# Optimization experiments

Measured on AMD Instinct MI355X. Metric: run time of the kernel, lower is better.

## Reference

```python
import jax, jax.numpy as jnp
import numpy as np
import math

# Config (matches init_kwargs)
B, IMG, NP, PS = 32, 224, 14, 16
P = PS * PS              # flattened patch dim = 256
D, NH, L, C = 768, 12, 12, 1000
DQ = D // NH             # 64
S = NP * NP + 1          # 197 tokens (cls + patches)
MLP_H = 4 * D
EPS = 1e-5


def positional_embeddings(seq_len, d):
    i = jnp.arange(seq_len, dtype=jnp.float32)[:, None]
    j = jnp.arange(d, dtype=jnp.float32)[None, :]
    even = jnp.sin(i / 10000.0 ** (j / d))
    odd = jnp.cos(i / 10000.0 ** ((j - 1.0) / d))
    return jnp.where(jnp.arange(d)[None, :] % 2 == 0, even, odd)


def layernorm(x, g, b):
    mu = jnp.mean(x, axis=-1, keepdims=True)
    var = jnp.mean((x - mu) ** 2, axis=-1, keepdims=True)
    return (x - mu) * jax.lax.rsqrt(var + EPS) * g + b


def setup_inputs() -> dict:
    key = jax.random.key(0)
    ks = jax.random.split(key, 24)
    s = 0.02
    return {
        "X": jax.random.normal(ks[0], (B, IMG, IMG), jnp.float32),
        "patch_W": jax.random.normal(ks[1], (P, D), jnp.float32) * s,
        "patch_b": jnp.zeros((D,), jnp.float32),
        "cls_token": jax.random.uniform(ks[2], (1, D), jnp.float32),
        "ln1_g": jnp.ones((L, D), jnp.float32),
        "ln1_b": jnp.zeros((L, D), jnp.float32),
        "Wq": jax.random.normal(ks[3], (L, NH, D, DQ), jnp.float32) * s,
        "bq": jnp.zeros((L, NH, DQ), jnp.float32),
        "Wk": jax.random.normal(ks[4], (L, NH, D, DQ), jnp.float32) * s,
        "bk": jnp.zeros((L, NH, DQ), jnp.float32),
        "Wv": jax.random.normal(ks[5], (L, NH, D, DQ), jnp.float32) * s,
        "bv": jnp.zeros((L, NH, DQ), jnp.float32),
        "proj_W": jax.random.normal(ks[6], (L, D, D), jnp.float32) * s,
        "proj_b": jnp.zeros((L, D), jnp.float32),
        "ln2_g": jnp.ones((L, D), jnp.float32),
        "ln2_b": jnp.zeros((L, D), jnp.float32),
        "mlp_W1": jax.random.normal(ks[7], (L, D, MLP_H), jnp.float32) * s,
        "mlp_b1": jnp.zeros((L, MLP_H), jnp.float32),
        "mlp_W2": jax.random.normal(ks[8], (L, MLP_H, D), jnp.float32) * s,
        "mlp_b2": jnp.zeros((L, D), jnp.float32),
        "head_W": jax.random.normal(ks[9], (D, C), jnp.float32) * s,
        "head_b": jnp.zeros((C,), jnp.float32),
    }


def _forward(X, patch_W, patch_b, cls_token, ln1_g, ln1_b, Wq, bq, Wk, bk, Wv, bv,
             proj_W, proj_b, ln2_g, ln2_b, mlp_W1, mlp_b1, mlp_W2, mlp_b2,
             head_W, head_b):
    b = X.shape[0]
    # patchify: (B,H,W) -> (B, NP*NP, PS*PS)
    patches = X.reshape(b, NP, PS, NP, PS).transpose(0, 1, 3, 2, 4).reshape(b, NP * NP, P)
    tok = patches @ patch_W + patch_b                      # (B, NP^2, D)
    cls = jnp.broadcast_to(cls_token[None], (b, 1, D))
    x = jnp.concatenate([cls, tok], axis=1)                # (B, S, D)
    x = x + positional_embeddings(S, D)[None]
    scale = 1.0 / math.sqrt(DQ)
    for l in range(L):
        n1 = layernorm(x, ln1_g[l], ln1_b[l])
        q = jnp.einsum("bsd,hde->bhse", n1, Wq[l]) + bq[l][None, :, None, :]
        k = jnp.einsum("bsd,hde->bhse", n1, Wk[l]) + bk[l][None, :, None, :]
        v = jnp.einsum("bsd,hde->bhse", n1, Wv[l]) + bv[l][None, :, None, :]
        att = jax.nn.softmax(jnp.einsum("bhse,bhte->bhst", q, k) * scale, axis=-1)
        o = jnp.einsum("bhst,bhte->bhse", att, v)          # (B,NH,S,DQ)
        o = o.transpose(0, 2, 1, 3).reshape(b, S, D)       # hstack heads
        x = x + o @ proj_W[l] + proj_b[l]
        n2 = layernorm(x, ln2_g[l], ln2_b[l])
        h = jax.nn.gelu(n2 @ mlp_W1[l] + mlp_b1[l], approximate=False)
        x = x + h @ mlp_W2[l] + mlp_b2[l]
    return x[:, 0] @ head_W + head_b                       # (B, C)


def reference(X, patch_W, patch_b, cls_token, ln1_g, ln1_b, Wq, bq, Wk, bk, Wv, bv,
              proj_W, proj_b, ln2_g, ln2_b, mlp_W1, mlp_b1, mlp_W2, mlp_b2,
              head_W, head_b):
    return _forward(X, patch_W, patch_b, cls_token, ln1_g, ln1_b, Wq, bq, Wk, bk,
                    Wv, bv, proj_W, proj_b, ln2_g, ln2_b, mlp_W1, mlp_b1,
                    mlp_W2, mlp_b2, head_W, head_b)
```

## Files before the change

kernel.cpp:

```cpp
#include <hip/hip_runtime.h>
#include <hip/hip_bf16.h>
#include <math.h>
#include <stdint.h>

#define VB   32
#define VS   197
#define VD   768
#define VNH  12
#define VDQ  64
#define VL   12
#define VMLP 3072
#define VC   1000
#define VP   256
#define VNPAT 196
#define VTOK (VB * VS)
#define TOKD ((size_t)VTOK * VD)

typedef __attribute__((ext_vector_type(4))) float f32x4;
typedef __attribute__((ext_vector_type(8))) short short8;

typedef __attribute__((address_space(1))) const unsigned int GU;
typedef __attribute__((address_space(3))) unsigned int LU;

__device__ __forceinline__ void gload_lds16(const void* g, void* l) {
    __builtin_amdgcn_global_load_lds((GU*)(uintptr_t)g, (LU*)(uintptr_t)l, 16, 0, 0);
}

__device__ __forceinline__ void xcd_swz(int gx, int gy, int& bx, int& by) {
    int nwg = gx * gy;
    int hw = by * gx + bx;
    int q = nwg >> 3, r = nwg & 7;
    int xcd = hw & 7, off = hw >> 3;
    int lid = (xcd < r ? xcd * (q + 1) : r * (q + 1) + (xcd - r) * q) + off;
    bx = lid % gx; by = lid / gx;
}

__device__ __forceinline__ float gelu_f(float x) {
    float t = 0.7978845608f * x * fmaf(0.044715f, x * x, 1.0f);
    float a = fminf(t * 2.8853900818f, 80.0f);
    float e = __builtin_amdgcn_exp2f(a);
    return x * e * __builtin_amdgcn_rcpf(1.0f + e);
}

__global__ void patchify_k(const float* __restrict__ X, __hip_bfloat16* __restrict__ P) {
    int idx = blockIdx.x * 256 + threadIdx.x;
    const int total = VB * VNPAT * VP;
    if (idx >= total) return;
    int i  = idx & 255;
    int p  = (idx >> 8) % VNPAT;
    int b  = (idx >> 8) / VNPAT;
    int pr = p / 14, pc = p % 14;
    int a  = i >> 4, c2 = i & 15;
    P[idx] = __float2bfloat16(X[((size_t)b * 224 + pr * 16 + a) * 224 + pc * 16 + c2]);
}

__global__ void pos_cls_k(float* __restrict__ x, const float* __restrict__ cls) {
    size_t idx = (size_t)blockIdx.x * 256 + threadIdx.x;
    if (idx >= TOKD) return;
    int j = (int)(idx % VD);
    int s = (int)((idx / VD) % VS);
    float jj = (float)(j & ~1);
    float freq = expf(-(jj / (float)VD) * 9.2103403719761836f);
    float ang  = (float)s * freq;
    float pe   = (j & 1) ? cosf(ang) : sinf(ang);
    if (s == 0) x[idx] = cls[j] + pe;
    else        x[idx] += pe;
}

__global__ __launch_bounds__(256) void layernorm_k(
    const float* __restrict__ x, __hip_bfloat16* __restrict__ y,
    const float* __restrict__ g, const float* __restrict__ bta)
{
    int t = blockIdx.x;
    const float* xr = x + (size_t)t * VD;
    __hip_bfloat16* yr = y + (size_t)t * VD;
    int tid = threadIdx.x;
    float v[3];
    float s = 0.f;
    #pragma unroll
    for (int i = 0; i < 3; i++) { v[i] = xr[tid + i * 256]; s += v[i]; }
    __shared__ float red[8];
    #pragma unroll
    for (int off = 32; off; off >>= 1) s += __shfl_xor(s, off);
    int lane = tid & 63, w = tid >> 6;
    if (!lane) red[w] = s;
    __syncthreads();
    float mu = (red[0] + red[1] + red[2] + red[3]) * (1.f / VD);
    float s2 = 0.f;
    #pragma unroll
    for (int i = 0; i < 3; i++) { float d0 = v[i] - mu; s2 += d0 * d0; }
    #pragma unroll
    for (int off = 32; off; off >>= 1) s2 += __shfl_xor(s2, off);
    if (!lane) red[4 + w] = s2;
    __syncthreads();
    float var = (red[4] + red[5] + red[6] + red[7]) * (1.f / VD);
    float rs = rsqrtf(var + 1e-5f);
    #pragma unroll
    for (int i = 0; i < 3; i++) {
        int j = tid + i * 256;
        yr[j] = __float2bfloat16((v[i] - mu) * rs * g[j] + bta[j]);
    }
}

template<int DO_LN>
__global__ __launch_bounds__(256) void combineln_k(
    float* __restrict__ x, const float* __restrict__ p0, const float* __restrict__ p1,
    const float* __restrict__ bias, const float* __restrict__ g,
    const float* __restrict__ bta, __hip_bfloat16* __restrict__ y)
{
    int t = blockIdx.x;
    size_t base = (size_t)t * VD;
    int tid = threadIdx.x;
    float v[3];
    float s = 0.f;
    #pragma unroll
    for (int i = 0; i < 3; i++) {
        int j = tid + i * 256;
        float val = x[base + j] + p0[base + j] + p1[base + j] + bias[j];
        x[base + j] = val;
        v[i] = val; s += val;
    }
    if (DO_LN) {
        __shared__ float red[8];
        #pragma unroll
        for (int off = 32; off; off >>= 1) s += __shfl_xor(s, off);
        int lane = tid & 63, w = tid >> 6;
        if (!lane) red[w] = s;
        __syncthreads();
        float mu = (red[0] + red[1] + red[2] + red[3]) * (1.f / VD);
        float s2 = 0.f;
        #pragma unroll
        for (int i = 0; i < 3; i++) { float d0 = v[i] - mu; s2 += d0 * d0; }
        #pragma unroll
        for (int off = 32; off; off >>= 1) s2 += __shfl_xor(s2, off);
        if (!lane) red[4 + w] = s2;
        __syncthreads();
        float var = (red[4] + red[5] + red[6] + red[7]) * (1.f / VD);
        float rs = rsqrtf(var + 1e-5f);
        #pragma unroll
        for (int i = 0; i < 3; i++) {
            int j = tid + i * 256;
            y[base + j] = __float2bfloat16((v[i] - mu) * rs * g[j] + bta[j]);
        }
    }
}

__global__ __launch_bounds__(256) void tpose_k(
    const float* __restrict__ in, __hip_bfloat16* __restrict__ out, int R, int C)
{
    __shared__ float t[32][33];
    int c0 = blockIdx.x * 32, r0 = blockIdx.y * 32;
    int tc = threadIdx.x & 31, tr = threadIdx.x >> 5;
    #pragma unroll
    for (int p = 0; p < 4; p++) {
        int r = r0 + tr + p * 8;
        t[tr + p * 8][tc] = (r < R && c0 + tc < C) ? in[(size_t)r * C + c0 + tc] : 0.f;
    }
    __syncthreads();
    #pragma unroll
    for (int p = 0; p < 4; p++) {
        int c = c0 + tr + p * 8;
        if (c < C && r0 + tc < R)
            out[(size_t)c * R + r0 + tc] = __float2bfloat16(t[tc][tr + p * 8]);
    }
}

#define OFF_PROJ (2304 * 768)
#define OFF_M1   (OFF_PROJ + 768 * 768)
#define OFF_M2   (OFF_M1 + 3072 * 768)

__device__ __forceinline__ unsigned pack2bf(float a, float b) {
    __hip_bfloat16 x = __float2bfloat16(a), y = __float2bfloat16(b);
    unsigned short ux = *(unsigned short*)&x, uy = *(unsigned short*)&y;
    return (unsigned)ux | ((unsigned)uy << 16);
}

__global__ __launch_bounds__(256) void wprep_k(
    const float* __restrict__ Wq, const float* __restrict__ Wk,
    const float* __restrict__ Wv, const float* __restrict__ Wp,
    const float* __restrict__ W1, const float* __restrict__ W2,
    __hip_bfloat16* __restrict__ wT)
{
    __shared__ float t[32][33];
    int z = blockIdx.x;
    const float* src; __hip_bfloat16* dst;
    int C, ldd, r0, c0;
    if (z < 1728) {
        int head = z / 48, tt = z % 48;
        int m = head / VNH, h = head % VNH;
        src = (m == 0 ? Wq : m == 1 ? Wk : Wv) + (size_t)h * VD * VDQ;
        dst = wT + ((size_t)m * VD + h * VDQ) * VD;
        C = VDQ; ldd = VD;
        r0 = (tt >> 1) * 32; c0 = (tt & 1) * 32;
    } else if (z < 2304) {
        int z2 = z - 1728;
        src = Wp; dst = wT + OFF_PROJ;
        C = VD; ldd = VD;
        r0 = (z2 / 24) * 32; c0 = (z2 % 24) * 32;
    } else if (z < 4608) {
        int z3 = z - 2304;
        src = W1; dst = wT + OFF_M1;
        C = VMLP; ldd = VD;
        r0 = (z3 / 96) * 32; c0 = (z3 % 96) * 32;
    } else {
        int z4 = z - 4608;
        src = W2; dst = wT + OFF_M2;
        C = VD; ldd = VMLP;
        r0 = (z4 / 24) * 32; c0 = (z4 % 24) * 32;
    }
    int tid = threadIdx.x;
    {
        int r = tid >> 3, cq = (tid & 7) << 2;
        float4 v = *(const float4*)&src[(size_t)(r0 + r) * C + c0 + cq];
        t[r][cq] = v.x; t[r][cq + 1] = v.y; t[r][cq + 2] = v.z; t[r][cq + 3] = v.w;
    }
    __syncthreads();
    {
        int c = tid >> 3, rq = (tid & 7) << 2;
        unsigned u0 = pack2bf(t[rq][c],     t[rq + 1][c]);
        unsigned u1 = pack2bf(t[rq + 2][c], t[rq + 3][c]);
        unsigned* dp = (unsigned*)&dst[(size_t)(c0 + c) * ldd + r0 + rq];
        dp[0] = u0; dp[1] = u1;
    }
}

__global__ void cball_k(const float* __restrict__ bq, const float* __restrict__ bk,
                        const float* __restrict__ bv, float* __restrict__ cb) {
    int idx = blockIdx.x * 256 + threadIdx.x;
    if (idx >= VL * 3 * VD) return;
    int l = idx / (3 * VD), n = idx % (3 * VD);
    int m = n / VD, wi = n % VD;
    const float* p = (m == 0) ? bq : (m == 1) ? bk : bv;
    cb[idx] = p[l * VD + wi];
}

__global__ void cls_k(const float* __restrict__ x, __hip_bfloat16* __restrict__ out) {
    int idx = blockIdx.x * 256 + threadIdx.x;
    if (idx >= VB * VD) return;
    int b = idx / VD, d = idx % VD;
    out[idx] = __float2bfloat16(x[(size_t)b * VS * VD + d]);
}

template<int EPI>
__global__ __launch_bounds__(256) void bgemm_k(
    const __hip_bfloat16* __restrict__ A,
    const __hip_bfloat16* __restrict__ BT,
    const float* __restrict__ bias,
    void* __restrict__ Co,
    int M, int K, int ldc, int Ncols)
{
    __shared__ short A_s[128][64];
    __shared__ short B_s[128][64];
    int bx = blockIdx.x, by = blockIdx.y;
    xcd_swz(gridDim.x, gridDim.y, bx, by);
    const int tid = threadIdx.x;
    const int w = tid >> 6, l = tid & 63;
    const int row0 = by * 128, col0 = bx * 128;
    const int wm = (w >> 1) << 6, wn = (w & 1) << 6;
    f32x4 acc[4][4] = {};

    const int lr = l >> 3;
    const int sslot = (l & 7) ^ lr;
    int arow[4], brow[4];
    #pragma unroll
    for (int i = 0; i < 4; i++) {
        int r = (4 * w + i) * 8 + lr;
        arow[i] = min(row0 + r, M - 1);
        brow[i] = min(col0 + r, Ncols - 1);
    }
    for (int k0 = 0; k0 < K; k0 += 64) {
        __syncthreads();
        #pragma unroll
        for (int i = 0; i < 4; i++) {
            int ch = 4 * w + i;
            gload_lds16((const void*)(A + (size_t)arow[i] * K + k0 + (sslot << 3)),
                        (void*)(&A_s[ch * 8][0]));
            gload_lds16((const void*)(BT + (size_t)brow[i] * K + k0 + (sslot << 3)),
                        (void*)(&B_s[ch * 8][0]));
        }
        __syncthreads();
        #pragma unroll
        for (int ks = 0; ks < 2; ks++) {
            const int s16 = (ks << 2) + (l >> 4);
            short8 av[4], bv[4];
            #pragma unroll
            for (int i = 0; i < 4; i++) {
                int ar = wm + i * 16 + (l & 15);
                av[i] = *(const short8*)((const char*)&A_s[ar][0] + ((s16 ^ (ar & 7)) << 4));
                int br = wn + i * 16 + (l & 15);
                bv[i] = *(const short8*)((const char*)&B_s[br][0] + ((s16 ^ (br & 7)) << 4));
            }
            #pragma unroll
            for (int i = 0; i < 4; i++)
                #pragma unroll
                for (int j = 0; j < 4; j++)
                    acc[i][j] = __builtin_amdgcn_mfma_f32_16x16x32_bf16(av[i], bv[j], acc[i][j], 0, 0, 0);
        }
    }
    const int rbase = row0 + wm + ((l >> 4) << 2);
    const int cbase = col0 + wn + (l & 15);
    #pragma unroll
    for (int i = 0; i < 4; i++) {
        #pragma unroll
        for (int q = 0; q < 4; q++) {
            int rr = rbase + i * 16 + q;
            if (rr >= M) continue;
            #pragma unroll
            for (int j = 0; j < 4; j++) {
                int c = cbase + j * 16;
                if (c >= Ncols) continue;
                float v = acc[i][j][q] + bias[c];
                if (EPI == 0) {
                    int orow = rr + rr / VNPAT + 1;
                    ((float*)Co)[(size_t)orow * ldc + c] = v;
                } else if (EPI == 1) {
                    ((__hip_bfloat16*)Co)[(size_t)rr * ldc + c] = __float2bfloat16(v);
                } else if (EPI == 2) {
                    ((float*)Co)[(size_t)rr * ldc + c] += v;
                } else if (EPI == 3) {
                    ((__hip_bfloat16*)Co)[(size_t)rr * ldc + c] = __float2bfloat16(gelu_f(v));
                } else {
                    ((float*)Co)[(size_t)rr * ldc + c] = v;
                }
            }
        }
    }
}

template<int EPI>
__global__ __launch_bounds__(512) void bgemm8_k(
    const __hip_bfloat16* __restrict__ A,
    const __hip_bfloat16* __restrict__ BT,
    const float* __restrict__ bias,
    __hip_bfloat16* __restrict__ Co,
    int M, int K, int ldc)
{
    __shared__ short SA[3][256][32];
    __shared__ short SB[3][256][32];
    const int tid = threadIdx.x;
    const int w = tid >> 6, l = tid & 63;
    const int fr = l & 15, g = l >> 4;
    const int wr = w >> 2, wc = w & 3;
    const int row0 = blockIdx.y * 256, col0 = blockIdx.x * 256;
    f32x4 acc[8][4] = {};

    const int sr = tid >> 2;
    const int sslot = (tid & 3) ^ ((sr >> 1) & 3);
    const __hip_bfloat16* aS[2]; const __hip_bfloat16* bS[2];
    #pragma unroll
    for (int u = 0; u < 2; u++) {
        aS[u] = A  + (size_t)min(row0 + u * 128 + sr, M - 1) * K + sslot * 8;
        bS[u] = BT + (size_t)(col0 + u * 128 + sr) * K + sslot * 8;
    }
    const int doff = sr * 64 + (tid & 3) * 16;

    #define STG_A(ring, t) { const int k0 = (t) << 5;                          \
        gload_lds16(aS[0] + k0, (char*)&SA[ring][0][0] + doff);                \
        gload_lds16(aS[1] + k0, (char*)&SA[ring][0][0] + 8192 + doff); }
    #define STG_B(ring, t) { const int k0 = (t) << 5;                          \
        gload_lds16(bS[0] + k0, (char*)&SB[ring][0][0] + doff);                \
        gload_lds16(bS[1] + k0, (char*)&SB[ring][0][0] + 8192 + doff); }

    const int nt = K >> 5;
    STG_A(0, 0); STG_B(0, 0);
    STG_A(1, 1); STG_B(1, 1);
    asm volatile("s_waitcnt vmcnt(4)" ::: "memory");
    __builtin_amdgcn_s_barrier();

    short8 breg[4];
    for (int t = 0; t < nt; t++) {
        const int ring = t % 3;
        const int rs   = (t + 2) % 3;
        const char* sa = (const char*)&SA[ring][0][0];
        const char* sb = (const char*)&SB[ring][0][0];
        short8 areg[4];
        #pragma unroll
        for (int n = 0; n < 4; n++) {
            int br = wc * 64 + n * 16 + fr;
            breg[n] = *(const short8*)(sb + br * 64 + ((g ^ ((br >> 1) & 3)) << 4));
        }
        #pragma unroll
        for (int m = 0; m < 4; m++) {
            int ar = wr * 128 + m * 16 + fr;
            areg[m] = *(const short8*)(sa + ar * 64 + ((g ^ ((ar >> 1) & 3)) << 4));
        }
        if (t + 2 < nt) STG_A(rs, t + 2);
        __builtin_amdgcn_s_barrier();
        asm volatile("s_waitcnt lgkmcnt(0)" ::: "memory");
        __builtin_amdgcn_sched_barrier(0);
        __builtin_amdgcn_s_setprio(1);
        #pragma unroll
        for (int m = 0; m < 4; m++)
            #pragma unroll
            for (int n = 0; n < 4; n++)
                acc[m][n] = __builtin_amdgcn_mfma_f32_16x16x32_bf16(areg[m], breg[n], acc[m][n], 0, 0, 0);
        __builtin_amdgcn_s_setprio(0);
        __builtin_amdgcn_s_barrier();
        #pragma unroll
        for (int m = 0; m < 4; m++) {
            int ar = wr * 128 + (m + 4) * 16 + fr;
            areg[m] = *(const short8*)(sa + ar * 64 + ((g ^ ((ar >> 1) & 3)) << 4));
        }
        if (t + 2 < nt) STG_B(rs, t + 2);
        __builtin_amdgcn_s_barrier();
        asm volatile("s_waitcnt lgkmcnt(0)" ::: "memory");
        __builtin_amdgcn_sched_barrier(0);
        __builtin_amdgcn_s_setprio(1);
        #pragma unroll
        for (int m = 0; m < 4; m++)
            #pragma unroll
            for (int n = 0; n < 4; n++)
                acc[m + 4][n] = __builtin_amdgcn_mfma_f32_16x16x32_bf16(areg[m], breg[n], acc[m + 4][n], 0, 0, 0);
        __builtin_amdgcn_s_setprio(0);
        if (t + 2 < nt) {
            asm volatile("s_waitcnt vmcnt(4)" ::: "memory");
            __builtin_amdgcn_s_barrier();
        } else if (t + 1 < nt) {
            asm volatile("s_waitcnt vmcnt(0)" ::: "memory");
            __builtin_amdgcn_s_barrier();
        }
    }
    #undef STG_A
    #undef STG_B

    const int rb = row0 + wr * 128 + (g << 2);
    const int cb = col0 + wc * 64 + fr;
    #pragma unroll
    for (int m = 0; m < 8; m++) {
        #pragma unroll
        for (int q = 0; q < 4; q++) {
            int rr = rb + m * 16 + q;
            if (rr >= M) continue;
            #pragma unroll
            for (int n = 0; n < 4; n++) {
                int c = cb + n * 16;
                float v = acc[m][n][q] + bias[c];
                if (EPI == 3) v = gelu_f(v);
                Co[(size_t)rr * ldc + c] = __float2bfloat16(v);
            }
        }
    }
}

__global__ __launch_bounds__(256) void bgemm5_k(
    const __hip_bfloat16* __restrict__ A,
    const __hip_bfloat16* __restrict__ BT,
    float* __restrict__ P,
    int M, int K, int ldc)
{
    __shared__ short A_s[128][64];
    __shared__ short B_s[128][64];
    int bx = blockIdx.x, by = blockIdx.y;
    xcd_swz(gridDim.x, gridDim.y, bx, by);
    const int ks = blockIdx.z;
    const int khalf = K >> 1;
    const __hip_bfloat16* Ab  = A  + (size_t)ks * khalf;
    const __hip_bfloat16* BTb = BT + (size_t)ks * khalf;
    float* Pb = P + (size_t)ks * TOKD;

    const int tid = threadIdx.x;
    const int w = tid >> 6, l = tid & 63;
    const int row0 = by * 128, col0 = bx * 128;
    const int wm = (w >> 1) << 6, wn = (w & 1) << 6;
    f32x4 acc[4][4] = {};

    const int lr = l >> 3;
    const int sslot = (l & 7) ^ lr;
    int arow[4], brow[4];
    #pragma unroll
    for (int i = 0; i < 4; i++) {
        int r = (4 * w + i) * 8 + lr;
        arow[i] = min(row0 + r, M - 1);
        brow[i] = col0 + r;
    }
    for (int k0 = 0; k0 < khalf; k0 += 64) {
        __syncthreads();
        #pragma unroll
        for (int i = 0; i < 4; i++) {
            int ch = 4 * w + i;
            gload_lds16((const void*)(Ab + (size_t)arow[i] * K + k0 + (sslot << 3)),
                        (void*)(&A_s[ch * 8][0]));
            gload_lds16((const void*)(BTb + (size_t)brow[i] * K + k0 + (sslot << 3)),
                        (void*)(&B_s[ch * 8][0]));
        }
        __syncthreads();
        #pragma unroll
        for (int ks2 = 0; ks2 < 2; ks2++) {
            const int s16 = (ks2 << 2) + (l >> 4);
            short8 av[4], bv[4];
            #pragma unroll
            for (int i = 0; i < 4; i++) {
                int ar = wm + i * 16 + (l & 15);
                av[i] = *(const short8*)((const char*)&A_s[ar][0] + ((s16 ^ (ar & 7)) << 4));
                int br = wn + i * 16 + (l & 15);
                bv[i] = *(const short8*)((const char*)&B_s[br][0] + ((s16 ^ (br & 7)) << 4));
            }
            #pragma unroll
            for (int i = 0; i < 4; i++)
                #pragma unroll
                for (int j = 0; j < 4; j++)
                    acc[i][j] = __builtin_amdgcn_mfma_f32_16x16x32_bf16(av[i], bv[j], acc[i][j], 0, 0, 0);
        }
    }
    const int rbase = row0 + wm + ((l >> 4) << 2);
    const int cbase = col0 + wn + (l & 15);
    #pragma unroll
    for (int i = 0; i < 4; i++) {
        #pragma unroll
        for (int q = 0; q < 4; q++) {
            int rr = rbase + i * 16 + q;
            if (rr >= M) continue;
            #pragma unroll
            for (int j = 0; j < 4; j++) {
                int c = cbase + j * 16;
                Pb[(size_t)rr * ldc + c] = acc[i][j][q];
            }
        }
    }
}

__device__ __forceinline__ int swz_idx(int row, int k) {
    return row * 256 + (((k >> 3) ^ (row & 7)) << 3) + (k & 7);
}

__global__ __launch_bounds__(256) void attn3_k(
    const __hip_bfloat16* __restrict__ qkv, __hip_bfloat16* __restrict__ o)
{
    __shared__ short V_t[64 * 256];
    __shared__ short P_s[4][16 * 256];
    const int half = blockIdx.x;
    const int bh = blockIdx.y;
    const int b = bh / VNH, h = bh % VNH;
    const int tid = threadIdx.x, w = tid >> 6, l = tid & 63;
    const int g = l >> 4, c16 = l & 15;

    const __hip_bfloat16* base = qkv + (size_t)(b * VS) * (3 * VD) + h * VDQ;

    {
        const __hip_bfloat16* vbase = base + 2 * VD;
        int t = tid & 31, e0 = (tid >> 5) * 8;
        #pragma unroll
        for (int it = 0; it < 7; it++) {
            int tt = it * 32 + t;
            if (tt < VS) {
                short8 vv = *(const short8*)(vbase + (size_t)tt * (3 * VD) + e0);
                #pragma unroll
                for (int j = 0; j < 8; j++) V_t[swz_idx(e0 + j, tt)] = vv[j];
            }
        }
        for (int idx = tid; idx < 64 * 27; idx += 256) {
            int e = idx / 27, k = 197 + idx % 27;
            V_t[swz_idx(e, k)] = 0;
        }
    }
    {
        unsigned* p0 = (unsigned*)&P_s[w][swz_idx(c16, 208 + g * 4)];
        p0[0] = 0; p0[1] = 0;
    }
    __syncthreads();

    const int qt_end = half ? 13 : 7;
    for (int qt = 7 * half + w; qt < qt_end; qt += 4) {
        const int q0 = qt * 16;
        int qr = min(q0 + c16, VS - 1);
        const __hip_bfloat16* qp = base + (size_t)qr * (3 * VD) + g * 8;
        short8 qa0 = *(const short8*)(qp);
        short8 qa1 = *(const short8*)(qp + 32);

        f32x4 st[13];
        __builtin_amdgcn_s_setprio(1);
        #pragma unroll
        for (int t = 0; t < 13; t++) {
            int kr = min(t * 16 + c16, VS - 1);
            const __hip_bfloat16* kp = base + VD + (size_t)kr * (3 * VD) + g * 8;
            short8 ka0 = *(const short8*)(kp);
            short8 ka1 = *(const short8*)(kp + 32);
            f32x4 z = {};
            z = __builtin_amdgcn_mfma_f32_16x16x32_bf16(ka0, qa0, z, 0, 0, 0);
            z = __builtin_amdgcn_mfma_f32_16x16x32_bf16(ka1, qa1, z, 0, 0, 0);
            st[t] = z;
        }
        __builtin_amdgcn_s_setprio(0);
        #pragma unroll
        for (int t = 0; t < 13; t++) {
            #pragma unroll
            for (int r = 0; r < 4; r++) {
                float v = st[t][r] * 0.125f;
                if (t == 12 && (4 * g + r) >= 5) v = -3.0e38f;
                st[t][r] = v;
            }
        }
        float m = -3.0e38f;
        #pragma unroll
        for (int t = 0; t < 13; t++)
            #pragma unroll
            for (int r = 0; r < 4; r++) m = fmaxf(m, st[t][r]);
        m = fmaxf(m, __shfl_xor(m, 16));
        m = fmaxf(m, __shfl_xor(m, 32));
        float sum = 0.f;
        #pragma unroll
        for (int t = 0; t < 13; t++)
            #pragma unroll
            for (int r = 0; r < 4; r++) { float e = expf(st[t][r] - m); st[t][r] = e; sum += e; }
        sum += __shfl_xor(sum, 16);
        sum += __shfl_xor(sum, 32);
        float inv = 1.f / sum;
        #pragma unroll
        for (int t = 0; t < 13; t++) {
            int k0 = 16 * t + 4 * g;
            unsigned* pp = (unsigned*)&P_s[w][swz_idx(c16, k0)];
            pp[0] = pack2bf(st[t][0] * inv, st[t][1] * inv);
            pp[1] = pack2bf(st[t][2] * inv, st[t][3] * inv);
        }
        f32x4 acc[4] = {};
        __builtin_amdgcn_s_setprio(1);
        #pragma unroll
        for (int ki = 0; ki < 7; ki++) {
            int k0 = ki * 32 + g * 8;
            short8 pa = *(const short8*)&P_s[w][swz_idx(c16, k0)];
            #pragma unroll
            for (int et = 0; et < 4; et++) {
                short8 vbf = *(const short8*)&V_t[swz_idx(et * 16 + c16, k0)];
                acc[et] = __builtin_amdgcn_mfma_f32_16x16x32_bf16(pa, vbf, acc[et], 0, 0, 0);
            }
        }
        __builtin_amdgcn_s_setprio(0);
        #pragma unroll
        for (int et = 0; et < 4; et++) {
            #pragma unroll
            for (int r = 0; r < 4; r++) {
                int q = q0 + 4 * g + r;
                if (q < VS)
                    o[((size_t)(b * VS) + q) * VD + h * VDQ + et * 16 + c16] =
                        __float2bfloat16(acc[et][r]);
            }
        }
    }
}

extern "C" void kernel_launch(void* const* d_in, const int* in_sizes, int n_in,
                              void* d_out, int out_size, void* d_ws, size_t ws_size,
                              hipStream_t stream) {
    (void)in_sizes; (void)n_in; (void)out_size; (void)ws_size;
    const float* X       = (const float*)d_in[0];
    const float* patch_W = (const float*)d_in[1];
    const float* patch_b = (const float*)d_in[2];
    const float* cls_tok = (const float*)d_in[3];
    const float* ln1_g   = (const float*)d_in[4];
    const float* ln1_b   = (const float*)d_in[5];
    const float* Wq      = (const float*)d_in[6];
    const float* bq      = (const float*)d_in[7];
    const float* Wk      = (const float*)d_in[8];
    const float* bk      = (const float*)d_in[9];
    const float* Wv      = (const float*)d_in[10];
    const float* bv      = (const float*)d_in[11];
    const float* proj_W  = (const float*)d_in[12];
    const float* proj_b  = (const float*)d_in[13];
    const float* ln2_g   = (const float*)d_in[14];
    const float* ln2_b   = (const float*)d_in[15];
    const float* mlp_W1  = (const float*)d_in[16];
    const float* mlp_b1  = (const float*)d_in[17];
    const float* mlp_W2  = (const float*)d_in[18];
    const float* mlp_b2  = (const float*)d_in[19];
    const float* head_W  = (const float*)d_in[20];
    const float* head_b  = (const float*)d_in[21];

    char* ws = (char*)d_ws;
    float*          x    = (float*)ws;
    __hip_bfloat16* tb   = (__hip_bfloat16*)(ws + 19365888);
    __hip_bfloat16* big  = (__hip_bfloat16*)(ws + 29048832);
    __hip_bfloat16* wT   = (__hip_bfloat16*)(ws + 67780608);
    float*          cbA  = (float*)(ws + 81936384);
    float*          pbuf = (float*)(ws + 82046976);

    cball_k<<<(VL * 3 * VD + 255) / 256, 256, 0, stream>>>(bq, bk, bv, cbA);

    patchify_k<<<(VB * VNPAT * VP + 255) / 256, 256, 0, stream>>>(X, big);
    {
        dim3 g(VD / 32, VP / 32);
        tpose_k<<<g, 256, 0, stream>>>(patch_W, wT, VP, VD);
    }
    {
        dim3 g(VD / 128, VB * VNPAT / 128);
        bgemm_k<0><<<g, 256, 0, stream>>>(big, wT, patch_b, x, VB * VNPAT, VP, VD, VD);
    }
    pos_cls_k<<<(unsigned)((TOKD + 255) / 256), 256, 0, stream>>>(x, cls_tok);

    const size_t WSZ = (size_t)VNH * VD * VDQ;
    for (int l = 0; l < VL; l++) {
        wprep_k<<<6912, 256, 0, stream>>>(
            Wq + l * WSZ, Wk + l * WSZ, Wv + l * WSZ,
            proj_W + (size_t)l * VD * VD,
            mlp_W1 + (size_t)l * VD * VMLP,
            mlp_W2 + (size_t)l * VMLP * VD, wT);

        if (l == 0)
            layernorm_k<<<VTOK, 256, 0, stream>>>(x, tb, ln1_g, ln1_b);

        {
            dim3 g(3 * VD / 256, (VTOK + 255) / 256);
            bgemm8_k<1><<<g, 512, 0, stream>>>(tb, wT, cbA + l * 3 * VD, big,
                                               VTOK, VD, 3 * VD);
        }
        {
            dim3 ga(2, VB * VNH);
            attn3_k<<<ga, 256, 0, stream>>>(big, tb);
        }
        {
            dim3 g(VD / 128, (VTOK + 127) / 128, 2);
            bgemm5_k<<<g, 256, 0, stream>>>(tb, wT + OFF_PROJ, pbuf, VTOK, VD, VD);
            combineln_k<1><<<VTOK, 256, 0, stream>>>(
                x, pbuf, pbuf + TOKD, proj_b + l * VD,
                ln2_g + l * VD, ln2_b + l * VD, tb);
        }
        {
            dim3 g(VMLP / 256, (VTOK + 255) / 256);
            bgemm8_k<3><<<g, 512, 0, stream>>>(tb, wT + OFF_M1, mlp_b1 + l * VMLP, big,
                                               VTOK, VD, VMLP);
        }
        {
            dim3 g(VD / 128, (VTOK + 127) / 128, 2);
            bgemm5_k<<<g, 256, 0, stream>>>(big, wT + OFF_M2, pbuf, VTOK, VMLP, VD);
            if (l + 1 < VL)
                combineln_k<1><<<VTOK, 256, 0, stream>>>(
                    x, pbuf, pbuf + TOKD, mlp_b2 + l * VD,
                    ln1_g + (l + 1) * VD, ln1_b + (l + 1) * VD, tb);
            else
                combineln_k<0><<<VTOK, 256, 0, stream>>>(
                    x, pbuf, pbuf + TOKD, mlp_b2 + l * VD,
                    nullptr, nullptr, nullptr);
        }
    }
    cls_k<<<(VB * VD + 255) / 256, 256, 0, stream>>>(x, tb);
    {
        dim3 gt((VC + 31) / 32, VD / 32);
        tpose_k<<<gt, 256, 0, stream>>>(head_W, wT, VD, VC);
        dim3 g((VC + 127) / 128, 1);
        bgemm_k<4><<<g, 256, 0, stream>>>(tb, wT, head_b, (float*)d_out,
                                          VB, VD, VC, VC);
    }
}
```

Before: 3.125 ms.

## Pipeline split-K GEMM with triple-buffered LDS ring and trim bgemm8 barriers

Replaces the single-buffered split-K GEMM used for the projection and MLP-down layers with a 3-stage ring of 32-wide K tiles, prefetched two steps ahead through direct global-to-LDS loads. A vmcnt-gated barrier replaces the two __syncthreads per step, so memory loads overlap MFMA work. Separately, three intra-iteration s_barriers are removed from the bgemm8 main loop to cut synchronisation stalls. Dropping those barriers relies on the ring spacing keeping LDS reads and writes apart, which adds a risk of races.

```diff
diff --git a/kernel.cpp b/kernel.cpp
--- a/kernel.cpp
+++ b/kernel.cpp
@@ -385,7 +385,6 @@
             areg[m] = *(const short8*)(sa + ar * 64 + ((g ^ ((ar >> 1) & 3)) << 4));
         }
         if (t + 2 < nt) STG_A(rs, t + 2);
-        __builtin_amdgcn_s_barrier();
         asm volatile("s_waitcnt lgkmcnt(0)" ::: "memory");
         __builtin_amdgcn_sched_barrier(0);
         __builtin_amdgcn_s_setprio(1);
@@ -395,14 +394,12 @@
             for (int n = 0; n < 4; n++)
                 acc[m][n] = __builtin_amdgcn_mfma_f32_16x16x32_bf16(areg[m], breg[n], acc[m][n], 0, 0, 0);
         __builtin_amdgcn_s_setprio(0);
-        __builtin_amdgcn_s_barrier();
         #pragma unroll
         for (int m = 0; m < 4; m++) {
             int ar = wr * 128 + (m + 4) * 16 + fr;
             areg[m] = *(const short8*)(sa + ar * 64 + ((g ^ ((ar >> 1) & 3)) << 4));
         }
         if (t + 2 < nt) STG_B(rs, t + 2);
-        __builtin_amdgcn_s_barrier();
         asm volatile("s_waitcnt lgkmcnt(0)" ::: "memory");
         __builtin_amdgcn_sched_barrier(0);
         __builtin_amdgcn_s_setprio(1);
@@ -442,14 +439,14 @@
     }
 }
 
-__global__ __launch_bounds__(256) void bgemm5_k(
+__global__ __launch_bounds__(256) void bgemm9_k(
     const __hip_bfloat16* __restrict__ A,
     const __hip_bfloat16* __restrict__ BT,
     float* __restrict__ P,
     int M, int K, int ldc)
 {
-    __shared__ short A_s[128][64];
-    __shared__ short B_s[128][64];
+    __shared__ short SA[3][128][32];
+    __shared__ short SB[3][128][32];
     int bx = blockIdx.x, by = blockIdx.y;
     xcd_swz(gridDim.x, gridDim.y, bx, by);
     const int ks = blockIdx.z;
@@ -460,50 +457,70 @@
 
     const int tid = threadIdx.x;
     const int w = tid >> 6, l = tid & 63;
+    const int fr = l & 15, g = l >> 4;
     const int row0 = by * 128, col0 = bx * 128;
     const int wm = (w >> 1) << 6, wn = (w & 1) << 6;
     f32x4 acc[4][4] = {};
 
-    const int lr = l >> 3;
-    const int sslot = (l & 7) ^ lr;
-    int arow[4], brow[4];
-    #pragma unroll
-    for (int i = 0; i < 4; i++) {
-        int r = (4 * w + i) * 8 + lr;
-        arow[i] = min(row0 + r, M - 1);
-        brow[i] = col0 + r;
-    }
-    for (int k0 = 0; k0 < khalf; k0 += 64) {
-        __syncthreads();
+    const __hip_bfloat16* aS[2]; const __hip_bfloat16* bS[2];
+    int doff[2];
+    #pragma unroll
+    for (int q = 0; q < 2; q++) {
+        int idx = tid + (q << 8);
+        int r = idx >> 2;
+        int s = (idx & 3) ^ ((r >> 1) & 3);
+        aS[q] = Ab  + (size_t)min(row0 + r, M - 1) * K + s * 8;
+        bS[q] = BTb + (size_t)(col0 + r) * K + s * 8;
+        doff[q] = idx << 4;
+    }
+
+    #define STG9(ring, t) { const int k0 = (t) << 5;                           \
+        gload_lds16(aS[0] + k0, (char*)&SA[ring][0][0] + doff[0]);             \
+        gload_lds16(aS[1] + k0, (char*)&SA[ring][0][0] + doff[1]);             \
+        gload_lds16(bS[0] + k0, (char*)&SB[ring][0][0] + doff[0]);             \
+        gload_lds16(bS[1] + k0, (char*)&SB[ring][0][0] + doff[1]); }
+
+    const int nt = khalf >> 5;
+    STG9(0, 0);
+    STG9(1, 1);
+    asm volatile("s_waitcnt vmcnt(4)" ::: "memory");
+    __builtin_amdgcn_s_barrier();
+
+    for (int t = 0; t < nt; t++) {
+        const int ring = t % 3;
+        const int rs   = (t + 2) % 3;
+        const char* sa = (const char*)&SA[ring][0][0];
+        const char* sb = (const char*)&SB[ring][0][0];
+        short8 av[4], bv[4];
         #pragma unroll
         for (int i = 0; i < 4; i++) {
-            int ch = 4 * w + i;
-            gload_lds16((const void*)(Ab + (size_t)arow[i] * K + k0 + (sslot << 3)),
-                        (void*)(&A_s[ch * 8][0]));
-            gload_lds16((const void*)(BTb + (size_t)brow[i] * K + k0 + (sslot << 3)),
-                        (void*)(&B_s[ch * 8][0]));
-        }
-        __syncthreads();
-        #pragma unroll
-        for (int ks2 = 0; ks2 < 2; ks2++) {
-            const int s16 = (ks2 << 2) + (l >> 4);
-            short8 av[4], bv[4];
-            #pragma unroll
-            for (int i = 0; i < 4; i++) {
-                int ar = wm + i * 16 + (l & 15);
-                av[i] = *(const short8*)((const char*)&A_s[ar][0] + ((s16 ^ (ar & 7)) << 4));
-                int br = wn + i * 16 + (l & 15);
-                bv[i] = *(const short8*)((const char*)&B_s[br][0] + ((s16 ^ (br & 7)) << 4));
-            }
-            #pragma unroll
-            for (int i = 0; i < 4; i++)
-                #pragma unroll
-                for (int j = 0; j < 4; j++)
-                    acc[i][j] = __builtin_amdgcn_mfma_f32_16x16x32_bf16(av[i], bv[j], acc[i][j], 0, 0, 0);
-        }
-    }
-    const int rbase = row0 + wm + ((l >> 4) << 2);
-    const int cbase = col0 + wn + (l & 15);
+            int ar = wm + i * 16 + fr;
+            av[i] = *(const short8*)(sa + ar * 64 + ((g ^ ((ar >> 1) & 3)) << 4));
+            int br = wn + i * 16 + fr;
+            bv[i] = *(const short8*)(sb + br * 64 + ((g ^ ((br >> 1) & 3)) << 4));
+        }
+        if (t + 2 < nt) STG9(rs, t + 2);
+        asm volatile("s_waitcnt lgkmcnt(0)" ::: "memory");
+        __builtin_amdgcn_sched_barrier(0);
+        __builtin_amdgcn_s_setprio(1);
+        #pragma unroll
+        for (int i = 0; i < 4; i++)
+            #pragma unroll
+            for (int j = 0; j < 4; j++)
+                acc[i][j] = __builtin_amdgcn_mfma_f32_16x16x32_bf16(av[i], bv[j], acc[i][j], 0, 0, 0);
+        __builtin_amdgcn_s_setprio(0);
+        if (t + 2 < nt) {
+            asm volatile("s_waitcnt vmcnt(4)" ::: "memory");
+            __builtin_amdgcn_s_barrier();
+        } else if (t + 1 < nt) {
+            asm volatile("s_waitcnt vmcnt(0)" ::: "memory");
+            __builtin_amdgcn_s_barrier();
+        }
+    }
+    #undef STG9
+
+    const int rbase = row0 + wm + (g << 2);
+    const int cbase = col0 + wn + fr;
     #pragma unroll
     for (int i = 0; i < 4; i++) {
         #pragma unroll
@@ -708,7 +725,7 @@
         }
         {
             dim3 g(VD / 128, (VTOK + 127) / 128, 2);
-            bgemm5_k<<<g, 256, 0, stream>>>(tb, wT + OFF_PROJ, pbuf, VTOK, VD, VD);
+            bgemm9_k<<<g, 256, 0, stream>>>(tb, wT + OFF_PROJ, pbuf, VTOK, VD, VD);
             combineln_k<1><<<VTOK, 256, 0, stream>>>(
                 x, pbuf, pbuf + TOKD, proj_b + l * VD,
                 ln2_g + l * VD, ln2_b + l * VD, tb);
@@ -720,7 +737,7 @@
         }
         {
             dim3 g(VD / 128, (VTOK + 127) / 128, 2);
-            bgemm5_k<<<g, 256, 0, stream>>>(big, wT + OFF_M2, pbuf, VTOK, VMLP, VD);
+            bgemm9_k<<<g, 256, 0, stream>>>(big, wT + OFF_M2, pbuf, VTOK, VMLP, VD);
             if (l + 1 < VL)
                 combineln_k<1><<<VTOK, 256, 0, stream>>>(
                     x, pbuf, pbuf + TOKD, mlp_b2 + l * VD,
```

Measured after the change: 2.797 ms. 10.5% less time.
